# Performance work log

Measured on AMD Instinct MI355X. Metric: run time of the kernel, lower is better.

The kernel has to match this reference:

```python
import jax, jax.numpy as jnp
import numpy as np

B, T, M = 64, 32, 64
IN_DIM, GNN, H, L = 256, 256, 4, 3
TEMP, OUT, NH, NLT = 256, 512, 8, 2
DIST_THR = 0.3


def _ln(x, s, b, eps=1e-5):
    mu = jnp.mean(x, -1, keepdims=True)
    v = jnp.mean(jnp.square(x - mu), -1, keepdims=True)
    return (x - mu) * jax.lax.rsqrt(v + eps) * s + b


def setup_inputs() -> dict:
    key = jax.random.key(0)
    ks = iter(jax.random.split(key, 64))
    def nrm(shape, scale=0.05):
        return jax.random.normal(next(ks), shape, jnp.float32) * scale
    C = GNN // H
    return dict(
        drone_feats=jax.random.normal(next(ks), (B, T, M, IN_DIM), jnp.float32),
        boxes=jax.random.uniform(next(ks), (B, T, M, 5), jnp.float32),
        drone_mask=jnp.ones((B, T, M), jnp.float32),
        in_proj_W=nrm((GNN, IN_DIM)), in_proj_b=jnp.zeros((GNN,), jnp.float32),
        gat_lin_W=nrm((L, GNN, GNN)), gat_edge_W=nrm((L, 3, GNN)),
        gat_att_src=nrm((L, H, C)), gat_att_dst=nrm((L, H, C)), gat_att_edge=nrm((L, H, C)),
        gat_bias=jnp.zeros((L, GNN), jnp.float32),
        gat_ln_s=jnp.ones((L, GNN), jnp.float32), gat_ln_b=jnp.zeros((L, GNN), jnp.float32),
        temp_W=nrm((TEMP, GNN)), temp_b=jnp.zeros((TEMP,), jnp.float32),
        pos_emb=nrm((1, T, TEMP), 0.02),
        qkv_W=nrm((NLT, 3 * TEMP, TEMP)), qkv_b=jnp.zeros((NLT, 3 * TEMP), jnp.float32),
        attn_out_W=nrm((NLT, TEMP, TEMP)), attn_out_b=jnp.zeros((NLT, TEMP), jnp.float32),
        ln1_s=jnp.ones((NLT, TEMP), jnp.float32), ln1_b=jnp.zeros((NLT, TEMP), jnp.float32),
        ln2_s=jnp.ones((NLT, TEMP), jnp.float32), ln2_b=jnp.zeros((NLT, TEMP), jnp.float32),
        ff1_W=nrm((NLT, 2 * TEMP, TEMP)), ff1_b=jnp.zeros((NLT, 2 * TEMP), jnp.float32),
        ff2_W=nrm((NLT, TEMP, 2 * TEMP)), ff2_b=jnp.zeros((NLT, TEMP), jnp.float32),
        pool_W=nrm((1, TEMP)), pool_b=jnp.zeros((1,), jnp.float32),
        out_W=nrm((OUT, TEMP)), out_b=jnp.zeros((OUT,), jnp.float32),
        out_ln_s=jnp.ones((OUT,), jnp.float32), out_ln_b=jnp.zeros((OUT,), jnp.float32),
    )


def reference(drone_feats, boxes, drone_mask, in_proj_W, in_proj_b, gat_lin_W, gat_edge_W,
              gat_att_src, gat_att_dst, gat_att_edge, gat_bias, gat_ln_s, gat_ln_b,
              temp_W, temp_b, pos_emb, qkv_W, qkv_b, attn_out_W, attn_out_b,
              ln1_s, ln1_b, ln2_s, ln2_b, ff1_W, ff1_b, ff2_W, ff2_b,
              pool_W, pool_b, out_W, out_b, out_ln_s, out_ln_b):
    Bv, Tv, Mv, _ = drone_feats.shape
    Hh, Cc = gat_att_src.shape[1], gat_att_src.shape[2]
    valid = drone_mask > 0.5                                  # [B,T,M]

    # ---- batched radius-graph build (dense masked form over tiny M) ----
    pos = boxes[..., 1:3]                                     # [B,T,M,2]
    rel = pos[..., None, :, :] - pos[..., :, None, :]         # [B,T,s,d,2] = pos_d - pos_s
    sq = jnp.sum(jnp.square(rel), -1)
    dist = jnp.sqrt(jnp.maximum(sq, 1e-12))                   # [B,T,s,d]
    eye = jnp.eye(Mv, dtype=bool)
    pair_valid = valid[..., :, None] & valid[..., None, :]
    adj = pair_valid & (dist < DIST_THR) & (~eye)             # real directed edges (s->d)
    eattr = jnp.where(adj[..., None], jnp.concatenate([dist[..., None], rel], -1), 0.0)
    # GATConv(add_self_loops=True, fill_value='mean'): self-loop attr = mean incoming attr
    deg = jnp.maximum(jnp.sum(adj, axis=-2), 1).astype(eattr.dtype)   # incoming per dst
    loop_attr = jnp.sum(eattr, axis=-3) / deg[..., None]              # [B,T,M,3]
    eattr = jnp.where(eye[:, :, None], loop_attr[..., None, :, :], eattr)
    full_adj = adj | (eye & pair_valid)

    # ---- spatial GAT stack ----
    x = jnp.einsum('btmi,gi->btmg', drone_feats, in_proj_W) + in_proj_b
    x = x * valid[..., None]
    for l in range(gat_lin_W.shape[0]):
        h = jnp.einsum('btmg,gk->btmk', x, gat_lin_W[l]).reshape(Bv, Tv, Mv, Hh, Cc)
        a_src = jnp.einsum('btmhc,hc->btmh', h, gat_att_src[l])
        a_dst = jnp.einsum('btmhc,hc->btmh', h, gat_att_dst[l])
        w_e = jnp.einsum('ehc,hc->eh', gat_edge_W[l].reshape(3, Hh, Cc), gat_att_edge[l])
        a_edge = jnp.einsum('btsde,eh->btsdh', eattr, w_e)
        logits = a_src[..., :, None, :] + a_dst[..., None, :, :] + a_edge
        logits = jnp.where(logits >= 0, logits, 0.2 * logits)        # LeakyReLU(0.2)
        logits = jnp.where(full_adj[..., None], logits, jnp.float32(-1e9))
        alpha = jax.nn.softmax(logits, axis=-3)                      # softmax over src per dst
        msg = jnp.einsum('btsdh,btshc->btdhc', alpha, h).reshape(Bv, Tv, Mv, Hh * Cc) + gat_bias[l]
        x = jax.nn.relu(_ln(msg + x, gat_ln_s[l], gat_ln_b[l]))

    nvalid = jnp.maximum(jnp.sum(valid, -1), 1).astype(x.dtype)
    frame = jnp.sum(x * valid[..., None], axis=-2) / nvalid[..., None]   # [B,T,GNN]

    # ---- temporal transformer (norm_first, relu, 2 layers) ----
    y = jnp.einsum('btg,dg->btd', frame, temp_W) + temp_b
    y = y + pos_emb[:, :Tv, :]
    D = y.shape[-1]
    hd = D // NH
    for l in range(qkv_W.shape[0]):
        z = _ln(y, ln1_s[l], ln1_b[l])
        qkv = z @ qkv_W[l].T + qkv_b[l]
        q, k, v = jnp.split(qkv, 3, axis=-1)
        q = q.reshape(Bv, Tv, NH, hd).transpose(0, 2, 1, 3)
        k = k.reshape(Bv, Tv, NH, hd).transpose(0, 2, 1, 3)
        v = v.reshape(Bv, Tv, NH, hd).transpose(0, 2, 1, 3)
        att = jax.nn.softmax(jnp.einsum('bhqd,bhkd->bhqk', q, k) / jnp.sqrt(jnp.float32(hd)), -1)
        o = jnp.einsum('bhqk,bhkd->bhqd', att, v).transpose(0, 2, 1, 3).reshape(Bv, Tv, D)
        y = y + o @ attn_out_W[l].T + attn_out_b[l]
        z = _ln(y, ln2_s[l], ln2_b[l])
        y = y + jax.nn.relu(z @ ff1_W[l].T + ff1_b[l]) @ ff2_W[l].T + ff2_b[l]

    wts = jax.nn.softmax(y @ pool_W.T + pool_b, axis=1)   # [B,T,1]
    pooled = jnp.sum(y * wts, axis=1)                     # [B,D]
    out = pooled @ out_W.T + out_b
    return jax.nn.relu(_ln(out, out_ln_s, out_ln_b))
```

## Files before the change

### kernel.cpp

```cpp
#include <hip/hip_runtime.h>
#include <math.h>

#define BT 2048

typedef __attribute__((ext_vector_type(8))) short bf16x8;
typedef __attribute__((ext_vector_type(4))) float f32x4;
typedef __attribute__((ext_vector_type(4))) unsigned short u16x4;

__device__ inline unsigned short f2bf(float f) {
    union { float f; unsigned u; } v; v.f = f;
    unsigned r = (v.u >> 16) & 1u;
    return (unsigned short)((v.u + 0x7FFFu + r) >> 16);
}
__device__ inline float bf2f(unsigned short s) {
    union { unsigned u; float f; } v; v.u = ((unsigned)s) << 16;
    return v.f;
}
__device__ inline float ubf(unsigned u) {
    union { unsigned u; float f; } v; v.u = u; return v.f;
}
__device__ inline unsigned cvt2(float a, float b) {
    unsigned r;
    asm("v_cvt_pk_bf16_f32 %0, %1, %2" : "=v"(r) : "v"(a), "v"(b));
    return r;
}

__device__ inline float dot4(const float4 a, const float4 b) {
    return fmaf(a.x, b.x, fmaf(a.y, b.y, fmaf(a.z, b.z, a.w * b.w)));
}

union F8 { float4 v2[2]; float f[8]; };

#define XP 264

__global__ __launch_bounds__(256) void k_prep(const float* __restrict__ inW,
                                              const float* __restrict__ gatW,
                                              unsigned short* __restrict__ dst) {
    int gid = blockIdx.x * 256 + threadIdx.x;
    int mat = gid >> 14;
    int r   = gid & 16383;
    int ks  = r >> 10;
    int nt  = (r >> 6) & 15;
    int lane = r & 63;
    int ln15 = lane & 15, q = lane >> 4;
    int n  = nt * 16 + ln15;
    int k0 = ks * 32 + q * 8;
    const float* src; bool tr;
    if (mat == 0) { src = inW; tr = true; }
    else          { src = gatW + (size_t)(mat - 1) * 65536; tr = false; }
    unsigned short* d = dst + ((size_t)mat * 16384 + r) * 16;
    if (ks < 8) {
        #pragma unroll
        for (int j = 0; j < 8; j++) {
            float v = tr ? src[n * 256 + k0 + j] : src[(size_t)(k0 + j) * 256 + n];
            unsigned short hi = f2bf(v);
            d[j]     = hi;
            d[8 + j] = f2bf(v - bf2f(hi));
        }
    } else {
        #pragma unroll
        for (int j = 0; j < 8; j++) { d[j] = 0; d[8 + j] = 0; }
    }
}

__global__ __launch_bounds__(64) void k_prep_aux(const float* __restrict__ gatW,
                                                 const float* __restrict__ attS,
                                                 const float* __restrict__ attD,
                                                 unsigned short* __restrict__ dst) {
    int l  = blockIdx.x >> 3;
    int ks = blockIdx.x & 7;
    int lane = threadIdx.x;
    int ln15 = lane & 15, q = lane >> 4;
    int k0 = ks * 32 + q * 8;
    const float* W = gatW + (size_t)l * 65536;
    unsigned short* d = dst + ((size_t)(l * 8 + ks) * 64 + lane) * 16;
    #pragma unroll
    for (int j = 0; j < 8; j++) {
        float v = 0.f;
        if (ln15 < 8) {
            int head = ln15 & 3;
            const float* a = (ln15 < 4 ? attS : attD) + (size_t)l * 256 + head * 64;
            const float* wr = W + (size_t)(k0 + j) * 256 + head * 64;
            for (int c = 0; c < 64; c++) v = fmaf(wr[c], a[c], v);
        }
        unsigned short hi = f2bf(v);
        d[j]     = hi;
        d[8 + j] = f2bf(v - bf2f(hi));
    }
}

__global__ __launch_bounds__(1024, 8) void k_gnn(const float* __restrict__ feats,
                                                 const float* __restrict__ boxes,
                                                 const float* __restrict__ maskp,
                                                 const unsigned short* __restrict__ BswAll,
                                                 const unsigned short* __restrict__ auxB,
                                                 const float* __restrict__ inb,
                                                 const float* __restrict__ edgeW,
                                                 const float* __restrict__ attEg,
                                                 const float* __restrict__ gbias,
                                                 const float* __restrict__ glns,
                                                 const float* __restrict__ glnb,
                                                 float* __restrict__ framebuf) {
    int bt = blockIdx.x;
    size_t fbase = (size_t)bt * 64 * 256;

    __shared__ __align__(16) unsigned short U[256 * 136];
    __shared__ float pxS[64], pyS[64], vmS[64];
    __shared__ float loopS[192];
    __shared__ float asrcS[4][64], adstS[4][64];
    __shared__ float wESall[36];
    __shared__ float sumsS[64][8];
    __shared__ float mrsS[64][2];
    __shared__ float nvS;

    unsigned short* xH = U;
    unsigned short* xL = U + 64 * XP;

    int tid = threadIdx.x, lane = tid & 63, w = tid >> 6;
    int ln15 = lane & 15, q = lane >> 4;
    int nt = w;
    int eh = w >> 2;
    int dq = w & 3;

    if (tid < 64) {
        const float* bx = boxes + (size_t)(bt * 64 + tid) * 5;
        pxS[tid] = bx[1];
        pyS[tid] = bx[2];
        vmS[tid] = maskp[bt * 64 + tid];
    } else if (tid < 100) {
        int idx = tid - 64;
        int l = idx / 12, r2 = idx - l * 12;
        int e = r2 >> 2, h2 = r2 & 3;
        float sm = 0.f;
        const float* ew = edgeW + (size_t)l * 768 + e * 256 + h2 * 64;
        const float* ae = attEg + (size_t)l * 256 + h2 * 64;
        for (int c = 0; c < 64; c++) sm += ew[c] * ae[c];
        wESall[idx] = sm;
    }
    #pragma unroll
    for (int j = 0; j < 4; j++) {
        int g = j * 4096 + tid * 4;
        int row = g >> 8, col = g & 255;
        float4 v4 = *(const float4*)&feats[fbase + g];
        unsigned p0 = cvt2(v4.x, v4.y);
        unsigned p1 = cvt2(v4.z, v4.w);
        float h0 = ubf(p0 << 16), h1 = ubf(p0 & 0xFFFF0000u);
        float h2 = ubf(p1 << 16), h3 = ubf(p1 & 0xFFFF0000u);
        unsigned l0 = cvt2(v4.x - h0, v4.y - h1);
        unsigned l1 = cvt2(v4.z - h2, v4.w - h3);
        *(unsigned*)&xH[row * XP + col]     = p0;
        *(unsigned*)&xH[row * XP + col + 2] = p1;
        *(unsigned*)&xL[row * XP + col]     = l0;
        *(unsigned*)&xL[row * XP + col + 2] = l1;
    }
    __syncthreads();

    {
        int d = tid >> 4, part = tid & 15;
        float pxd = pxS[d], pyd = pyS[d];
        bool vd = vmS[d] > 0.5f;
        float deg = 0.f, s0 = 0.f, s1 = 0.f, s2 = 0.f;
        #pragma unroll
        for (int k = 0; k < 4; k++) {
            int s = part * 4 + k;
            float rx = pxd - pxS[s], ry = pyd - pyS[s];
            float dist = sqrtf(fmaxf(rx * rx + ry * ry, 1e-12f));
            bool adj = vd && (vmS[s] > 0.5f) && (dist < 0.3f) && (s != d);
            if (adj) { deg += 1.f; s0 += dist; s1 += rx; s2 += ry; }
        }
        #pragma unroll
        for (int off = 1; off < 16; off <<= 1) {
            deg += __shfl_xor(deg, off);
            s0  += __shfl_xor(s0, off);
            s1  += __shfl_xor(s1, off);
            s2  += __shfl_xor(s2, off);
        }
        if (part == 0) {
            float dg = fmaxf(deg, 1.f);
            loopS[d * 3 + 0] = s0 / dg;
            loopS[d * 3 + 1] = s1 / dg;
            loopS[d * 3 + 2] = s2 / dg;
        }
    }
    if (tid == 0) {
        float nv = 0.f;
        for (int m = 0; m < 64; m++) nv += vmS[m] > 0.5f ? 1.f : 0.f;
        nvS = fmaxf(nv, 1.f);
    }

    {
        f32x4 acc[4];
        #pragma unroll
        for (int mt = 0; mt < 4; mt++) acc[mt] = (f32x4){0.f, 0.f, 0.f, 0.f};
        for (int ks = 0; ks < 8; ks++) {
            const unsigned short* fb = &BswAll[((size_t)(ks * 16 + nt) * 64 + lane) * 16];
            bf16x8 bhi = *(const bf16x8*)&fb[0];
            bf16x8 blo = *(const bf16x8*)&fb[8];
            #pragma unroll
            for (int mt = 0; mt < 4; mt++) {
                int ao = (mt * 16 + ln15) * XP + ks * 32 + q * 8;
                bf16x8 ahi = *(const bf16x8*)&xH[ao];
                bf16x8 alo = *(const bf16x8*)&xL[ao];
                acc[mt] = __builtin_amdgcn_mfma_f32_16x16x32_bf16(ahi, bhi, acc[mt], 0, 0, 0);
                acc[mt] = __builtin_amdgcn_mfma_f32_16x16x32_bf16(alo, bhi, acc[mt], 0, 0, 0);
                acc[mt] = __builtin_amdgcn_mfma_f32_16x16x32_bf16(ahi, blo, acc[mt], 0, 0, 0);
            }
        }
        __syncthreads();
        int c = nt * 16 + ln15;
        float bv = inb[c];
        #pragma unroll
        for (int mt = 0; mt < 4; mt++) {
            #pragma unroll
            for (int r = 0; r < 4; r++) {
                int m = mt * 16 + q * 4 + r;
                float v = (acc[mt][r] + bv) * (vmS[m] > 0.5f ? 1.f : 0.f);
                unsigned short hi = f2bf(v);
                xH[m * XP + c] = hi;
                xL[m * XP + c] = f2bf(v - bf2f(hi));
            }
        }
    }
    __syncthreads();

    for (int l = 0; l < 3; l++) {
        const unsigned short* BswL = BswAll + (size_t)(1 + l) * 16384 * 16;
        const float* biasl = gbias + (size_t)l * 256;
        const float* lnsl  = glns + (size_t)l * 256;
        const float* lnbl  = glnb + (size_t)l * 256;
        const float* wES   = wESall + l * 12;

        f32x4 acc[4];
        #pragma unroll
        for (int mt = 0; mt < 4; mt++) acc[mt] = (f32x4){0.f, 0.f, 0.f, 0.f};
        for (int ks = 0; ks < 8; ks++) {
            const unsigned short* fb = &BswL[((size_t)(ks * 16 + nt) * 64 + lane) * 16];
            bf16x8 bhi = *(const bf16x8*)&fb[0];
            bf16x8 blo = *(const bf16x8*)&fb[8];
            #pragma unroll
            for (int mt = 0; mt < 4; mt++) {
                int ao = (mt * 16 + ln15) * XP + ks * 32 + q * 8;
                bf16x8 ahi = *(const bf16x8*)&xH[ao];
                bf16x8 alo = *(const bf16x8*)&xL[ao];
                acc[mt] = __builtin_amdgcn_mfma_f32_16x16x32_bf16(ahi, bhi, acc[mt], 0, 0, 0);
                acc[mt] = __builtin_amdgcn_mfma_f32_16x16x32_bf16(alo, bhi, acc[mt], 0, 0, 0);
                acc[mt] = __builtin_amdgcn_mfma_f32_16x16x32_bf16(ahi, blo, acc[mt], 0, 0, 0);
            }
        }

        if (w >= 12) {
            int mm = w - 12;
            f32x4 aax = (f32x4){0.f, 0.f, 0.f, 0.f};
            const unsigned short* AuxL = auxB + (size_t)l * 8 * 64 * 16;
            for (int ks = 0; ks < 8; ks++) {
                const unsigned short* fb = &AuxL[((size_t)ks * 64 + lane) * 16];
                bf16x8 bhi = *(const bf16x8*)&fb[0];
                bf16x8 blo = *(const bf16x8*)&fb[8];
                int ao = (mm * 16 + ln15) * XP + ks * 32 + q * 8;
                bf16x8 ahi = *(const bf16x8*)&xH[ao];
                bf16x8 alo = *(const bf16x8*)&xL[ao];
                aax = __builtin_amdgcn_mfma_f32_16x16x32_bf16(ahi, bhi, aax, 0, 0, 0);
                aax = __builtin_amdgcn_mfma_f32_16x16x32_bf16(alo, bhi, aax, 0, 0, 0);
                aax = __builtin_amdgcn_mfma_f32_16x16x32_bf16(ahi, blo, aax, 0, 0, 0);
            }
            if (ln15 < 4) {
                #pragma unroll
                for (int r = 0; r < 4; r++) asrcS[ln15][mm * 16 + q * 4 + r] = aax[r];
            } else if (ln15 < 8) {
                #pragma unroll
                for (int r = 0; r < 4; r++) adstS[ln15 - 4][mm * 16 + q * 4 + r] = aax[r];
            }
        }

        f32x4 macc[4];
        #pragma unroll
        for (int ct = 0; ct < 4; ct++) {
            int c = eh * 64 + ct * 16 + ln15;
            float bv = biasl[c];
            #pragma unroll
            for (int r = 0; r < 4; r++) {
                int d2 = dq * 16 + q * 4 + r;
                int o = d2 * XP + c;
                macc[ct][r] = bf2f(xH[o]) + bf2f(xL[o]) + bv;
            }
        }
        __syncthreads();

        {
            int c = nt * 16 + ln15;
            #pragma unroll
            for (int mt = 0; mt < 4; mt++) {
                unsigned p0 = cvt2(acc[mt][0], acc[mt][1]);
                unsigned p1 = cvt2(acc[mt][2], acc[mt][3]);
                float h0 = ubf(p0 << 16), h1 = ubf(p0 & 0xFFFF0000u);
                float h2 = ubf(p1 << 16), h3 = ubf(p1 & 0xFFFF0000u);
                unsigned l0 = cvt2(acc[mt][0] - h0, acc[mt][1] - h1);
                unsigned l1 = cvt2(acc[mt][2] - h2, acc[mt][3] - h3);
                int s = mt * 16 + q * 4;
                *(unsigned*)&U[c * 136 + s]          = p0;
                *(unsigned*)&U[c * 136 + s + 2]      = p1;
                *(unsigned*)&U[c * 136 + 64 + s]     = l0;
                *(unsigned*)&U[c * 136 + 64 + s + 2] = l1;
            }
        }
        __syncthreads();

        {
            int d = dq * 16 + ln15;
            float pxd = pxS[d], pyd = pyS[d];
            bool vdv = vmS[d] > 0.5f;
            float adstv = adstS[eh][d];
            float lp0 = loopS[d * 3 + 0];
            float lp1 = loopS[d * 3 + 1];
            float lp2 = loopS[d * 3 + 2];
            float we0 = wES[eh], we1 = wES[4 + eh], we2 = wES[8 + eh];

            float lg[16];
            #pragma unroll
            for (int ks = 0; ks < 2; ks++) {
                int s0 = ks * 32 + q * 8;
                F8 PX, PY, VM, AS;
                PX.v2[0] = *(const float4*)&pxS[s0]; PX.v2[1] = *(const float4*)&pxS[s0 + 4];
                PY.v2[0] = *(const float4*)&pyS[s0]; PY.v2[1] = *(const float4*)&pyS[s0 + 4];
                VM.v2[0] = *(const float4*)&vmS[s0]; VM.v2[1] = *(const float4*)&vmS[s0 + 4];
                AS.v2[0] = *(const float4*)&asrcS[eh][s0];
                AS.v2[1] = *(const float4*)&asrcS[eh][s0 + 4];
                #pragma unroll
                for (int j = 0; j < 8; j++) {
                    int s = s0 + j;
                    float vsf = VM.f[j];
                    float rx = pxd - PX.f[j], ry = pyd - PY.f[j];
                    float dist = sqrtf(fmaxf(rx * rx + ry * ry, 1e-12f));
                    bool self = (s == d);
                    bool adj = vdv && (vsf > 0.5f) && (dist < 0.3f) && !self;
                    float e0 = adj ? dist : (self ? lp0 : 0.f);
                    float e1 = adj ? rx   : (self ? lp1 : 0.f);
                    float e2 = adj ? ry   : (self ? lp2 : 0.f);
                    bool fa = adj || (self && vdv);
                    float lv = AS.f[j] + adstv + e0 * we0 + e1 * we1 + e2 * we2;
                    lv = lv >= 0.f ? lv : 0.2f * lv;
                    lg[ks * 8 + j] = fa ? lv : -1e9f;
                }
            }

            float mx = lg[0];
            #pragma unroll
            for (int j = 1; j < 16; j++) mx = fmaxf(mx, lg[j]);
            mx = fmaxf(mx, __shfl_xor(mx, 16));
            mx = fmaxf(mx, __shfl_xor(mx, 32));
            float sm = 0.f;
            #pragma unroll
            for (int j = 0; j < 16; j++) { lg[j] = __expf(lg[j] - mx); sm += lg[j]; }
            sm += __shfl_xor(sm, 16);
            sm += __shfl_xor(sm, 32);
            float inv = 1.f / sm;

            bf16x8 ah[2], al[2];
            #pragma unroll
            for (int ks2 = 0; ks2 < 2; ks2++) {
                union { bf16x8 v; unsigned u[4]; } H, L;
                #pragma unroll
                for (int jj = 0; jj < 4; jj++) {
                    float a0 = lg[ks2 * 8 + jj * 2] * inv;
                    float a1 = lg[ks2 * 8 + jj * 2 + 1] * inv;
                    unsigned p = cvt2(a0, a1);
                    H.u[jj] = p;
                    float f0 = ubf(p << 16), f1 = ubf(p & 0xFFFF0000u);
                    L.u[jj] = cvt2(a0 - f0, a1 - f1);
                }
                ah[ks2] = H.v; al[ks2] = L.v;
            }

            #pragma unroll
            for (int ks2 = 0; ks2 < 2; ks2++) {
                #pragma unroll
                for (int ct = 0; ct < 4; ct++) {
                    const unsigned short* hb =
                        &U[(size_t)(eh * 64 + ct * 16 + ln15) * 136 + ks2 * 32 + q * 8];
                    bf16x8 bhi = *(const bf16x8*)&hb[0];
                    bf16x8 blo = *(const bf16x8*)&hb[64];
                    macc[ct] = __builtin_amdgcn_mfma_f32_16x16x32_bf16(ah[ks2], bhi, macc[ct], 0, 0, 0);
                    macc[ct] = __builtin_amdgcn_mfma_f32_16x16x32_bf16(al[ks2], bhi, macc[ct], 0, 0, 0);
                    macc[ct] = __builtin_amdgcn_mfma_f32_16x16x32_bf16(ah[ks2], blo, macc[ct], 0, 0, 0);
                }
            }
        }

        {
            float scv[4], bbv[4];
            #pragma unroll
            for (int ct = 0; ct < 4; ct++) {
                int c = eh * 64 + ct * 16 + ln15;
                scv[ct] = lnsl[c];
                bbv[ct] = lnbl[c];
            }
            float ps[4], ps2[4];
            #pragma unroll
            for (int r = 0; r < 4; r++) {
                float s = 0.f, s2 = 0.f;
                #pragma unroll
                for (int ct = 0; ct < 4; ct++) {
                    float v = macc[ct][r];
                    s += v; s2 += v * v;
                }
                ps[r] = s; ps2[r] = s2;
            }
            #pragma unroll
            for (int off = 1; off < 16; off <<= 1) {
                #pragma unroll
                for (int i = 0; i < 4; i++) {
                    ps[i]  += __shfl_xor(ps[i], off);
                    ps2[i] += __shfl_xor(ps2[i], off);
                }
            }
            if (ln15 == 0) {
                #pragma unroll
                for (int r = 0; r < 4; r++) {
                    int d2 = dq * 16 + q * 4 + r;
                    sumsS[d2][eh * 2 + 0] = ps[r];
                    sumsS[d2][eh * 2 + 1] = ps2[r];
                }
            }
            __syncthreads();
            if (tid < 64) {
                float S  = sumsS[tid][0] + sumsS[tid][2] + sumsS[tid][4] + sumsS[tid][6];
                float S2 = sumsS[tid][1] + sumsS[tid][3] + sumsS[tid][5] + sumsS[tid][7];
                float mu = S * (1.f / 256.f);
                float var = S2 * (1.f / 256.f) - mu * mu;
                mrsS[tid][0] = mu;
                mrsS[tid][1] = rsqrtf(var + 1e-5f);
            }
            __syncthreads();
            #pragma unroll
            for (int r = 0; r < 4; r++) {
                int d2 = dq * 16 + q * 4 + r;
                float mu = mrsS[d2][0], rs = mrsS[d2][1];
                #pragma unroll
                for (int ct = 0; ct < 4; ct++) {
                    float v = (macc[ct][r] - mu) * rs * scv[ct] + bbv[ct];
                    v = fmaxf(v, 0.f);
                    unsigned short hi = f2bf(v);
                    int o = d2 * XP + eh * 64 + ct * 16 + ln15;
                    xH[o] = hi;
                    xL[o] = f2bf(v - bf2f(hi));
                }
            }
        }
        __syncthreads();
    }

    if (tid < 256) {
        float s = 0.f;
        for (int m = 0; m < 64; m++) {
            float xv = bf2f(xH[m * XP + tid]) + bf2f(xL[m * XP + tid]);
            s += xv * (vmS[m] > 0.5f ? 1.f : 0.f);
        }
        framebuf[(size_t)bt * 256 + tid] = s / nvS;
    }
}

__global__ __launch_bounds__(256) void k_temp4(const float* __restrict__ framebuf,
                                               const float* __restrict__ tW,
                                               const float* __restrict__ tb,
                                               const float* __restrict__ pe,
                                               float* __restrict__ ybuf) {
    int b4 = blockIdx.x;
    int tid = threadIdx.x;
    __shared__ float frS[4][256];
    #pragma unroll
    for (int t = 0; t < 4; t++) frS[t][tid] = framebuf[(size_t)(b4 * 4 + t) * 256 + tid];
    __syncthreads();
    float acc[4];
    #pragma unroll
    for (int t = 0; t < 4; t++) acc[t] = tb[tid] + pe[((b4 * 4 + t) & 31) * 256 + tid];
    const float* wrow = tW + (size_t)tid * 256;
    for (int g = 0; g < 256; g += 4) {
        float4 wv = *(const float4*)&wrow[g];
        #pragma unroll
        for (int t = 0; t < 4; t++) acc[t] += dot4(*(const float4*)&frS[t][g], wv);
    }
    #pragma unroll
    for (int t = 0; t < 4; t++) ybuf[(size_t)(b4 * 4 + t) * 256 + tid] = acc[t];
}

__global__ __launch_bounds__(256) void k_ln_qkv4(const float* __restrict__ ybuf,
                                                 const float* __restrict__ ln_s,
                                                 const float* __restrict__ ln_b,
                                                 const float* __restrict__ qW,
                                                 const float* __restrict__ qb,
                                                 float* __restrict__ qkvbuf) {
    int b4 = blockIdx.x, tid = threadIdx.x;
    int lane = tid & 63, wv = tid >> 6;
    __shared__ float zS[4][256];
    {
        int bt = b4 * 4 + wv;
        float4 yv = *(const float4*)&ybuf[(size_t)bt * 256 + lane * 4];
        float s = yv.x + yv.y + yv.z + yv.w;
        float s2 = yv.x * yv.x + yv.y * yv.y + yv.z * yv.z + yv.w * yv.w;
        #pragma unroll
        for (int off = 1; off < 64; off <<= 1) { s += __shfl_xor(s, off); s2 += __shfl_xor(s2, off); }
        float mu = s * (1.f / 256.f);
        float var = s2 * (1.f / 256.f) - mu * mu;
        float rstd = rsqrtf(var + 1e-5f);
        float4 ls = *(const float4*)&ln_s[lane * 4];
        float4 lb = *(const float4*)&ln_b[lane * 4];
        float4 z;
        z.x = (yv.x - mu) * rstd * ls.x + lb.x;
        z.y = (yv.y - mu) * rstd * ls.y + lb.y;
        z.z = (yv.z - mu) * rstd * ls.z + lb.z;
        z.w = (yv.w - mu) * rstd * ls.w + lb.w;
        *(float4*)&zS[wv][lane * 4] = z;
    }
    __syncthreads();
    for (int r = 0; r < 3; r++) {
        int j = r * 256 + tid;
        float acc[4];
        float bv = qb[j];
        #pragma unroll
        for (int t = 0; t < 4; t++) acc[t] = bv;
        const float* wrow = qW + (size_t)j * 256;
        for (int i = 0; i < 256; i += 4) {
            float4 wv4 = *(const float4*)&wrow[i];
            #pragma unroll
            for (int t = 0; t < 4; t++) acc[t] += dot4(*(const float4*)&zS[t][i], wv4);
        }
        #pragma unroll
        for (int t = 0; t < 4; t++) qkvbuf[(size_t)(b4 * 4 + t) * 768 + j] = acc[t];
    }
}

__global__ __launch_bounds__(64) void k_attn(const float* __restrict__ qkvbuf,
                                             float* __restrict__ obuf) {
    int blk = blockIdx.x;
    int b = blk >> 3, h = blk & 7;
    int tid = threadIdx.x;
    __shared__ float Ks[32 * 32], Vs[32 * 32];
    for (int idx = tid; idx < 1024; idx += 64) {
        int tk = idx >> 5, c = idx & 31;
        size_t qbase = ((size_t)(b * 32 + tk)) * 768 + h * 32 + c;
        Ks[idx] = qkvbuf[qbase + 256];
        Vs[idx] = qkvbuf[qbase + 512];
    }
    __syncthreads();
    if (tid < 32) {
        int tq = tid;
        float qv[32];
        size_t qb0 = ((size_t)(b * 32 + tq)) * 768 + h * 32;
        #pragma unroll
        for (int c = 0; c < 32; c++) qv[c] = qkvbuf[qb0 + c];
        float scr[32];
        float mx = -1e30f;
        #pragma unroll
        for (int tk = 0; tk < 32; tk++) {
            float dd = 0.f;
            #pragma unroll
            for (int c = 0; c < 32; c++) dd = fmaf(qv[c], Ks[tk * 32 + c], dd);
            dd *= 0.17677669529663687f;
            scr[tk] = dd;
            mx = fmaxf(mx, dd);
        }
        float sm = 0.f;
        #pragma unroll
        for (int tk = 0; tk < 32; tk++) { scr[tk] = __expf(scr[tk] - mx); sm += scr[tk]; }
        float inv = 1.f / sm;
        float o[32];
        #pragma unroll
        for (int c = 0; c < 32; c++) o[c] = 0.f;
        #pragma unroll
        for (int tk = 0; tk < 32; tk++) {
            float a = scr[tk] * inv;
            #pragma unroll
            for (int c = 0; c < 32; c++) o[c] = fmaf(a, Vs[tk * 32 + c], o[c]);
        }
        size_t ob = ((size_t)(b * 32 + tq)) * 256 + h * 32;
        #pragma unroll
        for (int c = 0; c < 32; c++) obuf[ob + c] = o[c];
    }
}

__global__ __launch_bounds__(256) void k_attn_out4(const float* __restrict__ obuf,
                                                   const float* __restrict__ W,
                                                   const float* __restrict__ bvec,
                                                   float* __restrict__ ybuf) {
    int b4 = blockIdx.x, tid = threadIdx.x;
    int lane = tid & 63, wv = tid >> 6;
    __shared__ float oS[4][256];
    *(float4*)&oS[wv][lane * 4] = *(const float4*)&obuf[(size_t)(b4 * 4 + wv) * 256 + lane * 4];
    __syncthreads();
    float acc[4];
    float bv = bvec[tid];
    #pragma unroll
    for (int t = 0; t < 4; t++) acc[t] = bv;
    const float* wrow = W + (size_t)tid * 256;
    for (int i = 0; i < 256; i += 4) {
        float4 wv4 = *(const float4*)&wrow[i];
        #pragma unroll
        for (int t = 0; t < 4; t++) acc[t] += dot4(*(const float4*)&oS[t][i], wv4);
    }
    #pragma unroll
    for (int t = 0; t < 4; t++) ybuf[(size_t)(b4 * 4 + t) * 256 + tid] += acc[t];
}

__global__ __launch_bounds__(256) void k_ff4(float* __restrict__ ybuf,
                                             const float* __restrict__ ln_s,
                                             const float* __restrict__ ln_b,
                                             const float* __restrict__ W1,
                                             const float* __restrict__ b1,
                                             const float* __restrict__ W2,
                                             const float* __restrict__ b2) {
    int b4 = blockIdx.x, tid = threadIdx.x;
    int lane = tid & 63, wv = tid >> 6;
    __shared__ float zS[4][256];
    __shared__ float fS[4][512];
    {
        int bt = b4 * 4 + wv;
        float4 yv = *(const float4*)&ybuf[(size_t)bt * 256 + lane * 4];
        float s = yv.x + yv.y + yv.z + yv.w;
        float s2 = yv.x * yv.x + yv.y * yv.y + yv.z * yv.z + yv.w * yv.w;
        #pragma unroll
        for (int off = 1; off < 64; off <<= 1) { s += __shfl_xor(s, off); s2 += __shfl_xor(s2, off); }
        float mu = s * (1.f / 256.f);
        float var = s2 * (1.f / 256.f) - mu * mu;
        float rstd = rsqrtf(var + 1e-5f);
        float4 ls = *(const float4*)&ln_s[lane * 4];
        float4 lb = *(const float4*)&ln_b[lane * 4];
        float4 z;
        z.x = (yv.x - mu) * rstd * ls.x + lb.x;
        z.y = (yv.y - mu) * rstd * ls.y + lb.y;
        z.z = (yv.z - mu) * rstd * ls.z + lb.z;
        z.w = (yv.w - mu) * rstd * ls.w + lb.w;
        *(float4*)&zS[wv][lane * 4] = z;
    }
    __syncthreads();
    for (int r = 0; r < 2; r++) {
        int j = r * 256 + tid;
        float acc[4];
        float bv = b1[j];
        #pragma unroll
        for (int t = 0; t < 4; t++) acc[t] = bv;
        const float* wrow = W1 + (size_t)j * 256;
        for (int i = 0; i < 256; i += 4) {
            float4 wv4 = *(const float4*)&wrow[i];
            #pragma unroll
            for (int t = 0; t < 4; t++) acc[t] += dot4(*(const float4*)&zS[t][i], wv4);
        }
        #pragma unroll
        for (int t = 0; t < 4; t++) fS[t][j] = fmaxf(acc[t], 0.f);
    }
    __syncthreads();
    float acc[4];
    float bv = b2[tid];
    #pragma unroll
    for (int t = 0; t < 4; t++) acc[t] = bv;
    const float* wrow = W2 + (size_t)tid * 512;
    for (int jj = 0; jj < 512; jj += 4) {
        float4 wv4 = *(const float4*)&wrow[jj];
        #pragma unroll
        for (int t = 0; t < 4; t++) acc[t] += dot4(*(const float4*)&fS[t][jj], wv4);
    }
    #pragma unroll
    for (int t = 0; t < 4; t++) {
        size_t idx = (size_t)(b4 * 4 + t) * 256 + tid;
        ybuf[idx] = ybuf[idx] + acc[t];
    }
}

__global__ __launch_bounds__(256) void k_pool_out(const float* __restrict__ ybuf,
                                                  const float* __restrict__ pW,
                                                  const float* __restrict__ pb,
                                                  const float* __restrict__ oW,
                                                  const float* __restrict__ ob,
                                                  const float* __restrict__ lns,
                                                  const float* __restrict__ lnb,
                                                  float* __restrict__ dout) {
    int b = blockIdx.x, tid = threadIdx.x;
    __shared__ float redP[256];
    __shared__ float wS[32];
    __shared__ float pS[256];
    __shared__ float red[8];
    int tq = tid >> 3, part = tid & 7;
    float partial = 0.f;
    {
        const float* yrow = ybuf + ((size_t)(b * 32 + tq)) * 256 + part * 32;
        const float* pwp = pW + part * 32;
        #pragma unroll
        for (int j = 0; j < 32; j += 4) {
            float4 yv = *(const float4*)&yrow[j];
            float4 wv = *(const float4*)&pwp[j];
            partial += dot4(yv, wv);
        }
    }
    redP[tid] = partial;
    __syncthreads();
    if (tid < 32) {
        float s = pb[0];
        for (int p = 0; p < 8; p++) s += redP[tid * 8 + p];
        float mx = s;
        #pragma unroll
        for (int off = 16; off; off >>= 1) mx = fmaxf(mx, __shfl_xor(mx, off));
        float e = __expf(s - mx);
        float sm = e;
        #pragma unroll
        for (int off = 16; off; off >>= 1) sm += __shfl_xor(sm, off);
        wS[tid] = e / sm;
    }
    __syncthreads();
    float p = 0.f;
    for (int t = 0; t < 32; t++) p += ybuf[((size_t)(b * 32 + t)) * 256 + tid] * wS[t];
    pS[tid] = p;
    __syncthreads();
    float accs[2];
    for (int r = 0; r < 2; r++) {
        int j = r * 256 + tid;
        float acc = ob[j];
        const float* wrow = oW + (size_t)j * 256;
        for (int g = 0; g < 256; g += 4) {
            float4 pv = *(const float4*)&pS[g];
            float4 wv = *(const float4*)&wrow[g];
            acc += dot4(pv, wv);
        }
        accs[r] = acc;
    }
    float s = accs[0] + accs[1];
    float s2 = accs[0] * accs[0] + accs[1] * accs[1];
    #pragma unroll
    for (int off = 32; off; off >>= 1) {
        s += __shfl_xor(s, off);
        s2 += __shfl_xor(s2, off);
    }
    int wid = threadIdx.x >> 6;
    int lane = threadIdx.x & 63;
    if (lane == 0) { red[wid] = s; red[4 + wid] = s2; }
    __syncthreads();
    s = red[0] + red[1] + red[2] + red[3];
    s2 = red[4] + red[5] + red[6] + red[7];
    float mu = s * (1.f / 512.f);
    float var = s2 * (1.f / 512.f) - mu * mu;
    float rstd = rsqrtf(var + 1e-5f);
    dout[b * 512 + tid]       = fmaxf((accs[0] - mu) * rstd * lns[tid] + lnb[tid], 0.f);
    dout[b * 512 + tid + 256] = fmaxf((accs[1] - mu) * rstd * lns[tid + 256] + lnb[tid + 256], 0.f);
}

extern "C" void kernel_launch(void* const* d_in, const int* in_sizes, int n_in,
                              void* d_out, int out_size, void* d_ws, size_t ws_size,
                              hipStream_t stream) {
    const float* drone_feats = (const float*)d_in[0];
    const float* boxes       = (const float*)d_in[1];
    const float* drone_mask  = (const float*)d_in[2];
    const float* in_proj_W   = (const float*)d_in[3];
    const float* in_proj_b   = (const float*)d_in[4];
    const float* gat_lin_W   = (const float*)d_in[5];
    const float* gat_edge_W  = (const float*)d_in[6];
    const float* gat_att_src = (const float*)d_in[7];
    const float* gat_att_dst = (const float*)d_in[8];
    const float* gat_att_edge= (const float*)d_in[9];
    const float* gat_bias    = (const float*)d_in[10];
    const float* gat_ln_s    = (const float*)d_in[11];
    const float* gat_ln_b    = (const float*)d_in[12];
    const float* temp_W      = (const float*)d_in[13];
    const float* temp_b      = (const float*)d_in[14];
    const float* pos_emb     = (const float*)d_in[15];
    const float* qkv_W       = (const float*)d_in[16];
    const float* qkv_b       = (const float*)d_in[17];
    const float* attn_out_W  = (const float*)d_in[18];
    const float* attn_out_b  = (const float*)d_in[19];
    const float* ln1_s       = (const float*)d_in[20];
    const float* ln1_b       = (const float*)d_in[21];
    const float* ln2_s       = (const float*)d_in[22];
    const float* ln2_b       = (const float*)d_in[23];
    const float* ff1_W       = (const float*)d_in[24];
    const float* ff1_b       = (const float*)d_in[25];
    const float* ff2_W       = (const float*)d_in[26];
    const float* ff2_b       = (const float*)d_in[27];
    const float* pool_W      = (const float*)d_in[28];
    const float* pool_b      = (const float*)d_in[29];
    const float* out_W       = (const float*)d_in[30];
    const float* out_b       = (const float*)d_in[31];
    const float* out_ln_s    = (const float*)d_in[32];
    const float* out_ln_b    = (const float*)d_in[33];
    float* out = (float*)d_out;

    float* ws = (float*)d_ws;
    unsigned short* Bsw    = (unsigned short*)ws;
    unsigned short* BswAux = Bsw + (size_t)4 * 16384 * 16;
    size_t off = ((size_t)4 * 16384 * 16 + 3 * 8 * 64 * 16 + 1) / 2;
    float* framebuf = ws + off; off += (size_t)BT * 256;
    float* ybuf   = ws + off; off += (size_t)BT * 256;
    float* qkvbuf = ws + off; off += (size_t)BT * 768;
    float* obuf   = ws + off; off += (size_t)BT * 256;

    k_prep<<<dim3(256), dim3(256), 0, stream>>>(in_proj_W, gat_lin_W, Bsw);
    k_prep_aux<<<dim3(24), dim3(64), 0, stream>>>(gat_lin_W, gat_att_src, gat_att_dst, BswAux);
    k_gnn<<<dim3(BT), dim3(1024), 0, stream>>>(drone_feats, boxes, drone_mask, Bsw, BswAux,
        in_proj_b, gat_edge_W, gat_att_edge,
        gat_bias, gat_ln_s, gat_ln_b, framebuf);
    k_temp4<<<dim3(BT / 4), dim3(256), 0, stream>>>(framebuf, temp_W, temp_b, pos_emb, ybuf);
    for (int l = 0; l < 2; l++) {
        k_ln_qkv4<<<dim3(BT / 4), dim3(256), 0, stream>>>(ybuf, ln1_s + l * 256, ln1_b + l * 256,
            qkv_W + (size_t)l * 768 * 256, qkv_b + l * 768, qkvbuf);
        k_attn<<<dim3(512), dim3(64), 0, stream>>>(qkvbuf, obuf);
        k_attn_out4<<<dim3(BT / 4), dim3(256), 0, stream>>>(obuf,
            attn_out_W + (size_t)l * 65536, attn_out_b + l * 256, ybuf);
        k_ff4<<<dim3(BT / 4), dim3(256), 0, stream>>>(ybuf, ln2_s + l * 256, ln2_b + l * 256,
            ff1_W + (size_t)l * 131072, ff1_b + l * 512,
            ff2_W + (size_t)l * 131072, ff2_b + l * 256);
    }
    k_pool_out<<<dim3(64), dim3(256), 0, stream>>>(ybuf, pool_W, pool_b, out_W, out_b,
                                                   out_ln_s, out_ln_b, out);
}
```

Measured before the change: 1.142 ms.

## Replace temporal transformer FP32 GEMV kernels with generic split-bf16 MFMA GEMM

Replaces the per-4-row scalar FP32 dot-product kernels for the temporal projection, QKV, attention output and feed-forward layers with one generic tiled GEMM kernel. It uses bf16 MFMA with hi/lo splitting (three products) to keep near-FP32 accuracy, and fuses layernorm, bias, positional embedding, residual and ReLU into it. The weights are now reused across 64-row tiles instead of being re-read every 4 rows. The feed-forward is split into two launches through a new intermediate buffer, which adds extra global traffic and launches, and splitting the weights into hi/lo on the fly costs extra VALU work.

Result: faster. 965.3 us (-15.5%).

```diff
diff --git a/kernel.cpp b/kernel.cpp
--- a/kernel.cpp
+++ b/kernel.cpp
@@ -459,73 +459,132 @@
     }
 }
 
-__global__ __launch_bounds__(256) void k_temp4(const float* __restrict__ framebuf,
-                                               const float* __restrict__ tW,
-                                               const float* __restrict__ tb,
-                                               const float* __restrict__ pe,
-                                               float* __restrict__ ybuf) {
-    int b4 = blockIdx.x;
+#define TG_RELU 1
+#define TG_RES  2
+#define XPA 264
+__global__ __launch_bounds__(256, 4) void k_tgemm(const float* __restrict__ A,
+                                                  const float* __restrict__ lnS,
+                                                  const float* __restrict__ lnB,
+                                                  const float* __restrict__ W,
+                                                  const float* __restrict__ bias,
+                                                  const float* __restrict__ pe,
+                                                  float* __restrict__ out,
+                                                  int K, int N, int ldo, int flags) {
+    __shared__ __align__(16) unsigned short AH[64 * XPA];
+    __shared__ __align__(16) unsigned short AL[64 * XPA];
+
     int tid = threadIdx.x;
-    __shared__ float frS[4][256];
+    int lane = tid & 63, w = tid >> 6;
+    int ln15 = lane & 15, q = lane >> 4;
+    int Mbase = blockIdx.x * 64;
+    int Nbase = blockIdx.y * 64;
+    int r = tid >> 2, p = tid & 3;
+
+    f32x4 acc[4];
     #pragma unroll
-    for (int t = 0; t < 4; t++) frS[t][tid] = framebuf[(size_t)(b4 * 4 + t) * 256 + tid];
-    __syncthreads();
-    float acc[4];
+    for (int mt = 0; mt < 4; mt++) acc[mt] = (f32x4){0.f, 0.f, 0.f, 0.f};
+
+    int nchunks = K >> 8;
+    for (int kc = 0; kc < nchunks; kc++) {
+        {
+            const float* arow = A + (size_t)(Mbase + r) * K + kc * 256 + p * 4;
+            if (lnS && kc == 0) {
+                float s = 0.f, s2 = 0.f;
+                #pragma unroll
+                for (int j = 0; j < 16; j++) {
+                    float4 v = *(const float4*)&arow[j * 16];
+                    s  += v.x + v.y + v.z + v.w;
+                    s2 += v.x * v.x + v.y * v.y + v.z * v.z + v.w * v.w;
+                }
+                s  += __shfl_xor(s, 1);  s  += __shfl_xor(s, 2);
+                s2 += __shfl_xor(s2, 1); s2 += __shfl_xor(s2, 2);
+                float mu = s * (1.f / 256.f);
+                float var = s2 * (1.f / 256.f) - mu * mu;
+                float rstd = rsqrtf(var + 1e-5f);
+                #pragma unroll
+                for (int j = 0; j < 16; j++) {
+                    int c = p * 4 + j * 16;
+                    float4 v = *(const float4*)&arow[j * 16];
+                    float4 ls = *(const float4*)&lnS[c];
+                    float4 lb = *(const float4*)&lnB[c];
+                    float4 z;
+                    z.x = (v.x - mu) * rstd * ls.x + lb.x;
+                    z.y = (v.y - mu) * rstd * ls.y + lb.y;
+                    z.z = (v.z - mu) * rstd * ls.z + lb.z;
+                    z.w = (v.w - mu) * rstd * ls.w + lb.w;
+                    unsigned p0 = cvt2(z.x, z.y), p1 = cvt2(z.z, z.w);
+                    float f0 = ubf(p0 << 16), f1 = ubf(p0 & 0xFFFF0000u);
+                    float f2 = ubf(p1 << 16), f3 = ubf(p1 & 0xFFFF0000u);
+                    unsigned l0 = cvt2(z.x - f0, z.y - f1);
+                    unsigned l1 = cvt2(z.z - f2, z.w - f3);
+                    *(unsigned*)&AH[r * XPA + c]     = p0;
+                    *(unsigned*)&AH[r * XPA + c + 2] = p1;
+                    *(unsigned*)&AL[r * XPA + c]     = l0;
+                    *(unsigned*)&AL[r * XPA + c + 2] = l1;
+                }
+            } else {
+                #pragma unroll
+                for (int j = 0; j < 16; j++) {
+                    int c = p * 4 + j * 16;
+                    float4 v = *(const float4*)&arow[j * 16];
+                    unsigned p0 = cvt2(v.x, v.y), p1 = cvt2(v.z, v.w);
+                    float f0 = ubf(p0 << 16), f1 = ubf(p0 & 0xFFFF0000u);
+                    float f2 = ubf(p1 << 16), f3 = ubf(p1 & 0xFFFF0000u);
+                    unsigned l0 = cvt2(v.x - f0, v.y - f1);
+                    unsigned l1 = cvt2(v.z - f2, v.w - f3);
+                    *(unsigned*)&AH[r * XPA + c]     = p0;
+                    *(unsigned*)&AH[r * XPA + c + 2] = p1;
+                    *(unsigned*)&AL[r * XPA + c]     = l0;
+                    *(unsigned*)&AL[r * XPA + c + 2] = l1;
+                }
+            }
+        }
+        __syncthreads();
+
+        const float* wrow = W + (size_t)(Nbase + w * 16 + ln15) * K + kc * 256 + q * 8;
+        for (int ks = 0; ks < 8; ks++) {
+            float4 b0 = *(const float4*)&wrow[ks * 32];
+            float4 b1 = *(const float4*)&wrow[ks * 32 + 4];
+            unsigned h0 = cvt2(b0.x, b0.y), h1 = cvt2(b0.z, b0.w);
+            unsigned h2 = cvt2(b1.x, b1.y), h3 = cvt2(b1.z, b1.w);
+            float g0 = ubf(h0 << 16), g1 = ubf(h0 & 0xFFFF0000u);
+            float g2 = ubf(h1 << 16), g3 = ubf(h1 & 0xFFFF0000u);
+            float g4 = ubf(h2 << 16), g5 = ubf(h2 & 0xFFFF0000u);
+            float g6 = ubf(h3 << 16), g7 = ubf(h3 & 0xFFFF0000u);
+            union { bf16x8 v; unsigned u[4]; } BH, BL;
+            BH.u[0] = h0; BH.u[1] = h1; BH.u[2] = h2; BH.u[3] = h3;
+            BL.u[0] = cvt2(b0.x - g0, b0.y - g1);
+            BL.u[1] = cvt2(b0.z - g2, b0.w - g3);
+            BL.u[2] = cvt2(b1.x - g4, b1.y - g5);
+            BL.u[3] = cvt2(b1.z - g6, b1.w - g7);
+            bf16x8 bhi = BH.v, blo = BL.v;
+            #pragma unroll
+            for (int mt = 0; mt < 4; mt++) {
+                int ao = (mt * 16 + ln15) * XPA + ks * 32 + q * 8;
+                bf16x8 ahi = *(const bf16x8*)&AH[ao];
+                bf16x8 alo = *(const bf16x8*)&AL[ao];
+                acc[mt] = __builtin_amdgcn_mfma_f32_16x16x32_bf16(ahi, bhi, acc[mt], 0, 0, 0);
+                acc[mt] = __builtin_amdgcn_mfma_f32_16x16x32_bf16(alo, bhi, acc[mt], 0, 0, 0);
+                acc[mt] = __builtin_amdgcn_mfma_f32_16x16x32_bf16(ahi, blo, acc[mt], 0, 0, 0);
+            }
+        }
+        if (kc + 1 < nchunks) __syncthreads();
+    }
+
+    int n = Nbase + w * 16 + ln15;
+    float bv = bias[n];
     #pragma unroll
-    for (int t = 0; t < 4; t++) acc[t] = tb[tid] + pe[((b4 * 4 + t) & 31) * 256 + tid];
-    const float* wrow = tW + (size_t)tid * 256;
-    for (int g = 0; g < 256; g += 4) {
-        float4 wv = *(const float4*)&wrow[g];
-        #pragma unroll
-        for (int t = 0; t < 4; t++) acc[t] += dot4(*(const float4*)&frS[t][g], wv);
-    }
-    #pragma unroll
-    for (int t = 0; t < 4; t++) ybuf[(size_t)(b4 * 4 + t) * 256 + tid] = acc[t];
-}
-
-__global__ __launch_bounds__(256) void k_ln_qkv4(const float* __restrict__ ybuf,
-                                                 const float* __restrict__ ln_s,
-                                                 const float* __restrict__ ln_b,
-                                                 const float* __restrict__ qW,
-                                                 const float* __restrict__ qb,
-                                                 float* __restrict__ qkvbuf) {
-    int b4 = blockIdx.x, tid = threadIdx.x;
-    int lane = tid & 63, wv = tid >> 6;
-    __shared__ float zS[4][256];
-    {
-        int bt = b4 * 4 + wv;
-        float4 yv = *(const float4*)&ybuf[(size_t)bt * 256 + lane * 4];
-        float s = yv.x + yv.y + yv.z + yv.w;
-        float s2 = yv.x * yv.x + yv.y * yv.y + yv.z * yv.z + yv.w * yv.w;
-        #pragma unroll
-        for (int off = 1; off < 64; off <<= 1) { s += __shfl_xor(s, off); s2 += __shfl_xor(s2, off); }
-        float mu = s * (1.f / 256.f);
-        float var = s2 * (1.f / 256.f) - mu * mu;
-        float rstd = rsqrtf(var + 1e-5f);
-        float4 ls = *(const float4*)&ln_s[lane * 4];
-        float4 lb = *(const float4*)&ln_b[lane * 4];
-        float4 z;
-        z.x = (yv.x - mu) * rstd * ls.x + lb.x;
-        z.y = (yv.y - mu) * rstd * ls.y + lb.y;
-        z.z = (yv.z - mu) * rstd * ls.z + lb.z;
-        z.w = (yv.w - mu) * rstd * ls.w + lb.w;
-        *(float4*)&zS[wv][lane * 4] = z;
-    }
-    __syncthreads();
-    for (int r = 0; r < 3; r++) {
-        int j = r * 256 + tid;
-        float acc[4];
-        float bv = qb[j];
-        #pragma unroll
-        for (int t = 0; t < 4; t++) acc[t] = bv;
-        const float* wrow = qW + (size_t)j * 256;
-        for (int i = 0; i < 256; i += 4) {
-            float4 wv4 = *(const float4*)&wrow[i];
-            #pragma unroll
-            for (int t = 0; t < 4; t++) acc[t] += dot4(*(const float4*)&zS[t][i], wv4);
-        }
-        #pragma unroll
-        for (int t = 0; t < 4; t++) qkvbuf[(size_t)(b4 * 4 + t) * 768 + j] = acc[t];
+    for (int mt = 0; mt < 4; mt++) {
+        #pragma unroll
+        for (int rr = 0; rr < 4; rr++) {
+            int row = Mbase + mt * 16 + q * 4 + rr;
+            float v = acc[mt][rr] + bv;
+            if (pe) v += pe[(row & 31) * 256 + n];
+            size_t oidx = (size_t)row * ldo + n;
+            if (flags & TG_RES) v += out[oidx];
+            if (flags & TG_RELU) v = fmaxf(v, 0.f);
+            out[oidx] = v;
+        }
     }
 }
 
@@ -575,93 +634,6 @@
         size_t ob = ((size_t)(b * 32 + tq)) * 256 + h * 32;
         #pragma unroll
         for (int c = 0; c < 32; c++) obuf[ob + c] = o[c];
-    }
-}
-
-__global__ __launch_bounds__(256) void k_attn_out4(const float* __restrict__ obuf,
-                                                   const float* __restrict__ W,
-                                                   const float* __restrict__ bvec,
-                                                   float* __restrict__ ybuf) {
-    int b4 = blockIdx.x, tid = threadIdx.x;
-    int lane = tid & 63, wv = tid >> 6;
-    __shared__ float oS[4][256];
-    *(float4*)&oS[wv][lane * 4] = *(const float4*)&obuf[(size_t)(b4 * 4 + wv) * 256 + lane * 4];
-    __syncthreads();
-    float acc[4];
-    float bv = bvec[tid];
-    #pragma unroll
-    for (int t = 0; t < 4; t++) acc[t] = bv;
-    const float* wrow = W + (size_t)tid * 256;
-    for (int i = 0; i < 256; i += 4) {
-        float4 wv4 = *(const float4*)&wrow[i];
-        #pragma unroll
-        for (int t = 0; t < 4; t++) acc[t] += dot4(*(const float4*)&oS[t][i], wv4);
-    }
-    #pragma unroll
-    for (int t = 0; t < 4; t++) ybuf[(size_t)(b4 * 4 + t) * 256 + tid] += acc[t];
-}
-
-__global__ __launch_bounds__(256) void k_ff4(float* __restrict__ ybuf,
-                                             const float* __restrict__ ln_s,
-                                             const float* __restrict__ ln_b,
-                                             const float* __restrict__ W1,
-                                             const float* __restrict__ b1,
-                                             const float* __restrict__ W2,
-                                             const float* __restrict__ b2) {
-    int b4 = blockIdx.x, tid = threadIdx.x;
-    int lane = tid & 63, wv = tid >> 6;
-    __shared__ float zS[4][256];
-    __shared__ float fS[4][512];
-    {
-        int bt = b4 * 4 + wv;
-        float4 yv = *(const float4*)&ybuf[(size_t)bt * 256 + lane * 4];
-        float s = yv.x + yv.y + yv.z + yv.w;
-        float s2 = yv.x * yv.x + yv.y * yv.y + yv.z * yv.z + yv.w * yv.w;
-        #pragma unroll
-        for (int off = 1; off < 64; off <<= 1) { s += __shfl_xor(s, off); s2 += __shfl_xor(s2, off); }
-        float mu = s * (1.f / 256.f);
-        float var = s2 * (1.f / 256.f) - mu * mu;
-        float rstd = rsqrtf(var + 1e-5f);
-        float4 ls = *(const float4*)&ln_s[lane * 4];
-        float4 lb = *(const float4*)&ln_b[lane * 4];
-        float4 z;
-        z.x = (yv.x - mu) * rstd * ls.x + lb.x;
-        z.y = (yv.y - mu) * rstd * ls.y + lb.y;
-        z.z = (yv.z - mu) * rstd * ls.z + lb.z;
-        z.w = (yv.w - mu) * rstd * ls.w + lb.w;
-        *(float4*)&zS[wv][lane * 4] = z;
-    }
-    __syncthreads();
-    for (int r = 0; r < 2; r++) {
-        int j = r * 256 + tid;
-        float acc[4];
-        float bv = b1[j];
-        #pragma unroll
-        for (int t = 0; t < 4; t++) acc[t] = bv;
-        const float* wrow = W1 + (size_t)j * 256;
-        for (int i = 0; i < 256; i += 4) {
-            float4 wv4 = *(const float4*)&wrow[i];
-            #pragma unroll
-            for (int t = 0; t < 4; t++) acc[t] += dot4(*(const float4*)&zS[t][i], wv4);
-        }
-        #pragma unroll
-        for (int t = 0; t < 4; t++) fS[t][j] = fmaxf(acc[t], 0.f);
-    }
-    __syncthreads();
-    float acc[4];
-    float bv = b2[tid];
-    #pragma unroll
-    for (int t = 0; t < 4; t++) acc[t] = bv;
-    const float* wrow = W2 + (size_t)tid * 512;
-    for (int jj = 0; jj < 512; jj += 4) {
-        float4 wv4 = *(const float4*)&wrow[jj];
-        #pragma unroll
-        for (int t = 0; t < 4; t++) acc[t] += dot4(*(const float4*)&fS[t][jj], wv4);
-    }
-    #pragma unroll
-    for (int t = 0; t < 4; t++) {
-        size_t idx = (size_t)(b4 * 4 + t) * 256 + tid;
-        ybuf[idx] = ybuf[idx] + acc[t];
     }
 }
 
@@ -788,22 +760,31 @@
     float* ybuf   = ws + off; off += (size_t)BT * 256;
     float* qkvbuf = ws + off; off += (size_t)BT * 768;
     float* obuf   = ws + off; off += (size_t)BT * 256;
+    float* fbuf   = ws + off; off += (size_t)BT * 512;
 
     k_prep<<<dim3(256), dim3(256), 0, stream>>>(in_proj_W, gat_lin_W, Bsw);
     k_prep_aux<<<dim3(24), dim3(64), 0, stream>>>(gat_lin_W, gat_att_src, gat_att_dst, BswAux);
     k_gnn<<<dim3(BT), dim3(1024), 0, stream>>>(drone_feats, boxes, drone_mask, Bsw, BswAux,
         in_proj_b, gat_edge_W, gat_att_edge,
         gat_bias, gat_ln_s, gat_ln_b, framebuf);
-    k_temp4<<<dim3(BT / 4), dim3(256), 0, stream>>>(framebuf, temp_W, temp_b, pos_emb, ybuf);
+    k_tgemm<<<dim3(BT / 64, 4), dim3(256), 0, stream>>>(framebuf, nullptr, nullptr,
+        temp_W, temp_b, pos_emb, ybuf, 256, 256, 256, 0);
     for (int l = 0; l < 2; l++) {
-        k_ln_qkv4<<<dim3(BT / 4), dim3(256), 0, stream>>>(ybuf, ln1_s + l * 256, ln1_b + l * 256,
-            qkv_W + (size_t)l * 768 * 256, qkv_b + l * 768, qkvbuf);
+        k_tgemm<<<dim3(BT / 64, 12), dim3(256), 0, stream>>>(ybuf,
+            ln1_s + l * 256, ln1_b + l * 256,
+            qkv_W + (size_t)l * 768 * 256, qkv_b + l * 768, nullptr,
+            qkvbuf, 256, 768, 768, 0);
         k_attn<<<dim3(512), dim3(64), 0, stream>>>(qkvbuf, obuf);
-        k_attn_out4<<<dim3(BT / 4), dim3(256), 0, stream>>>(obuf,
-            attn_out_W + (size_t)l * 65536, attn_out_b + l * 256, ybuf);
-        k_ff4<<<dim3(BT / 4), dim3(256), 0, stream>>>(ybuf, ln2_s + l * 256, ln2_b + l * 256,
-            ff1_W + (size_t)l * 131072, ff1_b + l * 512,
-            ff2_W + (size_t)l * 131072, ff2_b + l * 256);
+        k_tgemm<<<dim3(BT / 64, 4), dim3(256), 0, stream>>>(obuf, nullptr, nullptr,
+            attn_out_W + (size_t)l * 65536, attn_out_b + l * 256, nullptr,
+            ybuf, 256, 256, 256, TG_RES);
+        k_tgemm<<<dim3(BT / 64, 8), dim3(256), 0, stream>>>(ybuf,
+            ln2_s + l * 256, ln2_b + l * 256,
+            ff1_W + (size_t)l * 131072, ff1_b + l * 512, nullptr,
+            fbuf, 256, 512, 512, TG_RELU);
+        k_tgemm<<<dim3(BT / 64, 4), dim3(256), 0, stream>>>(fbuf, nullptr, nullptr,
+            ff2_W + (size_t)l * 131072, ff2_b + l * 256, nullptr,
+            ybuf, 512, 256, 256, TG_RES);
     }
     k_pool_out<<<dim3(64), dim3(256), 0, stream>>>(ybuf, pool_W, pool_b, out_W, out_b,
                                                    out_ln_s, out_ln_b, out);
```
